# Optimization experiments

Measured on AMD Instinct MI355X. Metric: run time of the kernel, lower is better.

Reference implementation:

```python
import jax, jax.numpy as jnp
import numpy as np

TOP_K = 2
N_EXP = 64
EVAL_CAPACITY = 2.0


def setup_inputs() -> dict:
    key = jax.random.key(0)
    k1, k2 = jax.random.split(key)
    x = jax.random.normal(k1, (4, 4096, 2048), dtype=jnp.float32)
    w_g = jax.random.normal(k2, (N_EXP, 2048), dtype=jnp.float32) * 0.02  # Linear(n_embd, n_exp, bias=False)
    return {"x": x, "w_g": w_g}


def reference(x, w_g):
    B, T, C = x.shape
    num_tokens = B * T
    x_flat = x.reshape(num_tokens, C)
    # gating logits: [N, E]
    logits = jnp.einsum('nc,ec->ne', x_flat, w_g)
    # top-k selection
    top_k_logits, top_k_indices = jax.lax.top_k(logits, TOP_K)  # [N, k]
    router_probs = jax.nn.softmax(top_k_logits, axis=-1)        # [N, k]
    # static expert capacity (eval path)
    exp_capacity = max(int(TOP_K * EVAL_CAPACITY * num_tokens / N_EXP), 4)
    # one-hot expert mask [N, k, E]
    expert_mask = jax.nn.one_hot(top_k_indices, N_EXP, dtype=jnp.int32)
    # rank tokens within each expert via cumsum over (k-major, token) order
    reshaped = expert_mask.transpose(1, 0, 2).reshape(TOP_K * num_tokens, N_EXP)
    cumsum = jnp.cumsum(reshaped, axis=0)
    position = cumsum.reshape(TOP_K, num_tokens, N_EXP).transpose(1, 0, 2)  # [N, k, E]
    rank = (position - 1) * expert_mask
    capacity_mask = (rank < exp_capacity).astype(jnp.int32)
    final_mask = expert_mask * capacity_mask                     # [N, k, E]
    probs_mask = (final_mask.sum(axis=-1) > 0)                   # [N, k] bool
    router_probs_masked = router_probs * probs_mask.astype(router_probs.dtype)
    final_rank = rank.sum(axis=-1)                               # [N, k]
    return final_mask, router_probs_masked, top_k_indices, final_rank, exp_capacity
```

## Files before the change

### kernel.cpp

```cpp
#include <hip/hip_runtime.h>
#include <math.h>

#define C_DIM 2048
#define E_DIM 64
#define KC    128
#define BT    16
#define NW    4

typedef _Float16 h4    __attribute__((ext_vector_type(4)));
typedef _Float16 v8hf  __attribute__((ext_vector_type(8)));
typedef float    f32x4 __attribute__((ext_vector_type(4)));

#define SCALE      64.0f
#define INV_SCALE2 (1.0f/4096.0f)

__launch_bounds__(256)
__global__ void k_wsplit(const float* __restrict__ w, _Float16* __restrict__ wfrag)
{
    int t  = blockIdx.x * 256 + threadIdx.x;
    int l  = t & 63;
    int ni = (t >> 6) & 3;
    int q  = t >> 8;
    int e  = 16 * ni + (l & 15);
    int k0 = 32 * q + (l >> 4) * 8;
    const float* src = w + (size_t)e * C_DIM + k0;
    float4 a = *(const float4*)(src);
    float4 b = *(const float4*)(src + 4);
    float s[8] = {a.x, a.y, a.z, a.w, b.x, b.y, b.z, b.w};
    v8hf hv, lv;
#pragma unroll
    for (int j = 0; j < 8; ++j) {
        float sc = s[j] * SCALE;
        _Float16 h = (_Float16)sc;
        hv[j] = h;
        lv[j] = (_Float16)(sc - (float)h);
    }
    size_t fo = (size_t)(q * 4 + ni) * 2 * 512;
    *(v8hf*)(wfrag + fo + l * 8)       = hv;
    *(v8hf*)(wfrag + fo + 512 + l * 8) = lv;
}

__launch_bounds__(256, 4)
__global__ void k_logits_top2(const float* __restrict__ x, const _Float16* __restrict__ wfrag,
                              unsigned char* __restrict__ idx0, unsigned char* __restrict__ idx1,
                              float* __restrict__ dlt, unsigned short* __restrict__ gcounts,
                              int nblk)
{
    __shared__ alignas(16) char smem[2 * BT * KC * 2];

    const int tid  = threadIdx.x;
    const int lane = tid & 63;
    const int wk   = tid >> 6;
    const int ln15 = lane & 15;
    const int g    = lane >> 4;
    const int t0   = blockIdx.x * BT;

    f32x4 acc[4];
#pragma unroll
    for (int ni = 0; ni < 4; ++ni) acc[ni] = (f32x4)0.0f;

    float4 xr[2];

#define LOADX(kb)                                                              \
    {                                                                          \
        _Pragma("unroll")                                                      \
        for (int r = 0; r < 2; ++r) {                                          \
            int i = tid + 256 * r;                                             \
            int row = i >> 5, c4 = i & 31;                                     \
            xr[r] = *(const float4*)(x + (size_t)(t0 + row) * C_DIM + (kb) + c4 * 4); \
        }                                                                      \
    }

#define STOREX()                                                               \
    {                                                                          \
        _Pragma("unroll")                                                      \
        for (int r = 0; r < 2; ++r) {                                          \
            int i = tid + 256 * r;                                             \
            int row = i >> 5, c4 = i & 31;                                     \
            float4 v = xr[r];                                                  \
            float s0 = v.x * SCALE, s1 = v.y * SCALE, s2 = v.z * SCALE, s3 = v.w * SCALE; \
            _Float16 h0 = (_Float16)s0, h1 = (_Float16)s1, h2 = (_Float16)s2, h3 = (_Float16)s3; \
            h4 hv = {h0, h1, h2, h3};                                          \
            h4 lv = {(_Float16)(s0 - (float)h0), (_Float16)(s1 - (float)h1),   \
                     (_Float16)(s2 - (float)h2), (_Float16)(s3 - (float)h3)};  \
            int boff = row * 256 + ((c4 * 8) ^ ((row & 7) << 4));              \
            *(h4*)(smem + boff) = hv;                                          \
            *(h4*)(smem + 4096 + boff) = lv;                                   \
        }                                                                      \
    }

    LOADX(0);
    STOREX();
    __syncthreads();

    const int aoff = ln15 * 256 + (((wk << 6) + (g << 4)) ^ ((ln15 & 7) << 4));

    for (int c = 0; c < 16; ++c) {
        if (c < 15) LOADX((c + 1) * KC);

        const char* wp = (const char*)wfrag + ((size_t)(4 * c + wk) << 13) + (lane << 4);
        v8hf bh[4], bl[4];
#pragma unroll
        for (int ni = 0; ni < 4; ++ni) {
            bh[ni] = *(const v8hf*)(wp + (size_t)(2 * ni) * 1024);
            bl[ni] = *(const v8hf*)(wp + (size_t)(2 * ni) * 1024 + 1024);
        }
        v8hf ah = *(const v8hf*)(smem + aoff);
        v8hf al = *(const v8hf*)(smem + 4096 + aoff);

#pragma unroll
        for (int ni = 0; ni < 4; ++ni) {
            acc[ni] = __builtin_amdgcn_mfma_f32_16x16x32_f16(ah, bh[ni], acc[ni], 0, 0, 0);
            acc[ni] = __builtin_amdgcn_mfma_f32_16x16x32_f16(ah, bl[ni], acc[ni], 0, 0, 0);
            acc[ni] = __builtin_amdgcn_mfma_f32_16x16x32_f16(al, bh[ni], acc[ni], 0, 0, 0);
        }

        __syncthreads();
        if (c < 15) STOREX();
        __syncthreads();
    }

    float* lgs = (float*)smem;
    int*   cnt = (int*)(smem + 4096);
    if (tid < 128) cnt[tid] = 0;
#pragma unroll
    for (int w = 0; w < NW; ++w) {
        if (wk == w) {
#pragma unroll
            for (int ni = 0; ni < 4; ++ni)
#pragma unroll
                for (int gg = 0; gg < 4; ++gg) {
                    int row = (g << 2) + gg;
                    int e   = 16 * ni + ln15;
                    float vv = acc[ni][gg] * INV_SCALE2;
                    if (w == 0) lgs[row * 64 + e]  = vv;
                    else        lgs[row * 64 + e] += vv;
                }
        }
        __syncthreads();
    }

#pragma unroll
    for (int t = 0; t < 4; ++t) {
        int rowl = (wk << 2) + t;
        float v = lgs[rowl * 64 + lane];
        float vv = v; int ix = lane;
#pragma unroll
        for (int off = 32; off > 0; off >>= 1) {
            float ov = __shfl_down(vv, off, 64);
            int   oi = __shfl_down(ix, off, 64);
            if (ov > vv || (ov == vv && oi < ix)) { vv = ov; ix = oi; }
        }
        int   i1 = __shfl(ix, 0, 64);
        float v1 = __shfl(vv, 0, 64);

        vv = (lane == i1) ? -3.0e38f : v; ix = lane;
#pragma unroll
        for (int off = 32; off > 0; off >>= 1) {
            float ov = __shfl_down(vv, off, 64);
            int   oi = __shfl_down(ix, off, 64);
            if (ov > vv || (ov == vv && oi < ix)) { vv = ov; ix = oi; }
        }
        int   i2 = __shfl(ix, 0, 64);
        float v2 = __shfl(vv, 0, 64);

        if (lane == 0) {
            int n = t0 + rowl;
            idx0[n] = (unsigned char)i1;
            idx1[n] = (unsigned char)i2;
            dlt[n]  = v2 - v1;
            atomicAdd(&cnt[i1], 1);
            atomicAdd(&cnt[64 + i2], 1);
        }
    }

    __syncthreads();
    if (tid < 128) {
        int e = tid & 63, k = tid >> 6;
        gcounts[(size_t)e * (2 * nblk) + k * nblk + blockIdx.x] = (unsigned short)cnt[tid];
    }
}

__launch_bounds__(64)
__global__ void k_scan2(unsigned short* __restrict__ g, int S)
{
    const int e = blockIdx.x, lane = threadIdx.x;
    unsigned short* row = g + (size_t)e * S;
    int vals[32];
    const int R = S >> 6;
#pragma unroll
    for (int r = 0; r < 32; ++r) if (r < R) vals[r] = row[(r << 6) + lane];
    int running = 0;
#pragma unroll
    for (int r = 0; r < 32; ++r) {
        if (r >= R) break;
        int v = vals[r], s = v;
#pragma unroll
        for (int off = 1; off < 64; off <<= 1) {
            int t = __shfl_up(s, off, 64);
            if (lane >= off) s += t;
        }
        row[(r << 6) + lane] = (unsigned short)(s - v + running);
        running += __shfl(s, 63, 64);
    }
}

__launch_bounds__(128)
__global__ void k_rank_out(const unsigned char* __restrict__ idx0, const unsigned char* __restrict__ idx1,
                           const unsigned short* __restrict__ gpre, const float* __restrict__ dlt,
                           float* __restrict__ out, int N, int cap, int nblk)
{
    const int b = blockIdx.x, tid = threadIdx.x;
    const int lane = tid & 63, kk = tid >> 6;
    const int t0 = b * BT;
    __shared__ int sm_ix[2][BT], sm_rk[2][BT];

    int v = -1, base = 0;
    if (lane < BT) {
        v = (kk ? idx1 : idx0)[t0 + lane];
        base = gpre[(size_t)v * (2 * nblk) + kk * nblk + b];
    }
    const unsigned long long ltm = (1ull << lane) - 1ull;
    int pre = 0;
    for (int e = 0; e < 64; ++e) {
        unsigned long long bb = __ballot(v == e);
        if (v == e) pre = __popcll(bb & ltm);
    }
    if (lane < BT) { sm_ix[kk][lane] = v; sm_rk[kk][lane] = base + pre; }
    __syncthreads();

#pragma unroll
    for (int rep = 0; rep < 4; ++rep) {
        int f   = tid + 128 * rep;
        int n2  = f >> 5;
        int rem = (f & 31) * 4;
        int kq  = rem >> 6;
        int e0  = rem & 63;
        int ix  = sm_ix[kq][n2];
        int rr  = sm_rk[kq][n2];
        float val = (rr < cap) ? 1.0f : 0.0f;
        float4 o = make_float4(0.f, 0.f, 0.f, 0.f);
        int d = ix - e0;
        if (d >= 0 && d < 4) ((float*)&o)[d] = val;
        *(float4*)(out + (size_t)(t0 + n2) * 128 + rem) = o;
    }

    size_t B = (size_t)2 * N * E_DIM;
    if (tid < 2 * BT) {
        int n2 = tid >> 1, kq = tid & 1;
        int n  = t0 + n2;
        int gi = 2 * n + kq;
        int ix = sm_ix[kq][n2];
        int rr = sm_rk[kq][n2];
        float d  = dlt[n];
        float e1 = expf(d);
        float inv = 1.0f / (1.0f + e1);
        float p  = kq ? (e1 * inv) : inv;
        bool keep = rr < cap;
        out[B + gi]         = keep ? p : 0.0f;
        out[B + 2 * N + gi] = (float)ix;
        out[B + 4 * N + gi] = (float)rr;
    }
    if (b == 0 && tid == 0) out[B + 6 * N] = (float)cap;
}

extern "C" void kernel_launch(void* const* d_in, const int* in_sizes, int n_in,
                              void* d_out, int out_size, void* d_ws, size_t ws_size,
                              hipStream_t stream)
{
    const float* x  = (const float*)d_in[0];
    const float* wg = (const float*)d_in[1];
    const int N = in_sizes[0] / C_DIM;
    const int nblk = N / BT;

    char* ws = (char*)d_ws;
    unsigned char*  idx0    = (unsigned char*)ws;
    unsigned char*  idx1    = idx0 + N;
    float*          dlt     = (float*)(idx1 + N);
    unsigned short* gcounts = (unsigned short*)(dlt + N);
    _Float16*       wfrag   = (_Float16*)(gcounts + (size_t)64 * 2 * nblk);

    float* out = (float*)d_out;

    int cap = (int)((long long)2 * 2 * N / E_DIM);
    if (cap < 4) cap = 4;

    k_wsplit<<<64, 256, 0, stream>>>(wg, wfrag);
    k_logits_top2<<<nblk, 256, 0, stream>>>(x, wfrag, idx0, idx1, dlt, gcounts, nblk);
    k_scan2<<<E_DIM, 64, 0, stream>>>(gcounts, 2 * nblk);
    k_rank_out<<<nblk, 128, 0, stream>>>(idx0, idx1, gcounts, dlt, out, N, cap, nblk);
}
```

Baseline: 251.3 us.

## Double tokens per block, double-buffer LDS and prefetch weight fragments

Raises the token tile per block from 16 to 32, so each wave runs two M-subtiles that share the same weight fragments, halving weight reloads per token. The LDS staging buffer is now double-buffered, which removes one barrier per K-chunk, and the next chunk's weight fragments are prefetched into registers while the current chunk computes. The downstream scan and output kernels are resized to the new block count. The costs are higher register and LDS use, with the occupancy hint dropped from launch bounds, and half as many blocks in the grid.

```diff
diff --git a/kernel.cpp b/kernel.cpp
--- a/kernel.cpp
+++ b/kernel.cpp
@@ -4,7 +4,7 @@
 #define C_DIM 2048
 #define E_DIM 64
 #define KC    128
-#define BT    16
+#define BT    32
 #define NW    4
 
 typedef _Float16 h4    __attribute__((ext_vector_type(4)));
@@ -35,18 +35,18 @@
         hv[j] = h;
         lv[j] = (_Float16)(sc - (float)h);
     }
-    size_t fo = (size_t)(q * 4 + ni) * 2 * 512;
+    size_t fo = (size_t)(q * 4 + ni) * 1024;
     *(v8hf*)(wfrag + fo + l * 8)       = hv;
     *(v8hf*)(wfrag + fo + 512 + l * 8) = lv;
 }
 
-__launch_bounds__(256, 4)
+__launch_bounds__(256)
 __global__ void k_logits_top2(const float* __restrict__ x, const _Float16* __restrict__ wfrag,
                               unsigned char* __restrict__ idx0, unsigned char* __restrict__ idx1,
                               float* __restrict__ dlt, unsigned short* __restrict__ gcounts,
                               int nblk)
 {
-    __shared__ alignas(16) char smem[2 * BT * KC * 2];
+    __shared__ alignas(16) char smem[2 * 16384];
 
     const int tid  = threadIdx.x;
     const int lane = tid & 63;
@@ -55,94 +55,112 @@
     const int g    = lane >> 4;
     const int t0   = blockIdx.x * BT;
 
-    f32x4 acc[4];
-#pragma unroll
-    for (int ni = 0; ni < 4; ++ni) acc[ni] = (f32x4)0.0f;
-
-    float4 xr[2];
-
-#define LOADX(kb)                                                              \
-    {                                                                          \
-        _Pragma("unroll")                                                      \
-        for (int r = 0; r < 2; ++r) {                                          \
-            int i = tid + 256 * r;                                             \
-            int row = i >> 5, c4 = i & 31;                                     \
+    f32x4 acc[2][4];
+#pragma unroll
+    for (int mi = 0; mi < 2; ++mi)
+#pragma unroll
+        for (int ni = 0; ni < 4; ++ni) acc[mi][ni] = (f32x4)0.0f;
+
+    float4 xr[4];
+    v8hf bh[2][4], bl[2][4];
+
+#define LOADX(kb)                                                               \
+    {                                                                           \
+        _Pragma("unroll")                                                       \
+        for (int r = 0; r < 4; ++r) {                                           \
+            int i = tid + 256 * r;                                              \
+            int row = i >> 5, c4 = i & 31;                                      \
             xr[r] = *(const float4*)(x + (size_t)(t0 + row) * C_DIM + (kb) + c4 * 4); \
-        }                                                                      \
-    }
-
-#define STOREX()                                                               \
-    {                                                                          \
-        _Pragma("unroll")                                                      \
-        for (int r = 0; r < 2; ++r) {                                          \
-            int i = tid + 256 * r;                                             \
-            int row = i >> 5, c4 = i & 31;                                     \
-            float4 v = xr[r];                                                  \
+        }                                                                       \
+    }
+
+#define STOREX(bf)                                                              \
+    {                                                                           \
+        _Pragma("unroll")                                                       \
+        for (int r = 0; r < 4; ++r) {                                           \
+            int i = tid + 256 * r;                                              \
+            int row = i >> 5, c4 = i & 31;                                      \
+            float4 v = xr[r];                                                   \
             float s0 = v.x * SCALE, s1 = v.y * SCALE, s2 = v.z * SCALE, s3 = v.w * SCALE; \
             _Float16 h0 = (_Float16)s0, h1 = (_Float16)s1, h2 = (_Float16)s2, h3 = (_Float16)s3; \
-            h4 hv = {h0, h1, h2, h3};                                          \
-            h4 lv = {(_Float16)(s0 - (float)h0), (_Float16)(s1 - (float)h1),   \
-                     (_Float16)(s2 - (float)h2), (_Float16)(s3 - (float)h3)};  \
-            int boff = row * 256 + ((c4 * 8) ^ ((row & 7) << 4));              \
-            *(h4*)(smem + boff) = hv;                                          \
-            *(h4*)(smem + 4096 + boff) = lv;                                   \
-        }                                                                      \
+            h4 hv = {h0, h1, h2, h3};                                           \
+            h4 lv = {(_Float16)(s0 - (float)h0), (_Float16)(s1 - (float)h1),    \
+                     (_Float16)(s2 - (float)h2), (_Float16)(s3 - (float)h3)};   \
+            int boff = (bf) * 16384 + row * 256 + ((c4 * 8) ^ ((row & 7) << 4));\
+            *(h4*)(smem + boff)        = hv;                                    \
+            *(h4*)(smem + boff + 8192) = lv;                                    \
+        }                                                                       \
+    }
+
+#define LOADB(c, s)                                                             \
+    {                                                                           \
+        const char* wp = (const char*)wfrag + ((size_t)(4 * (c) + wk) << 13) + (lane << 4); \
+        _Pragma("unroll")                                                       \
+        for (int ni = 0; ni < 4; ++ni) {                                        \
+            bh[s][ni] = *(const v8hf*)(wp + ni * 2048);                         \
+            bl[s][ni] = *(const v8hf*)(wp + ni * 2048 + 1024);                  \
+        }                                                                       \
     }
 
     LOADX(0);
-    STOREX();
+    LOADB(0, 0);
+    STOREX(0);
     __syncthreads();
 
-    const int aoff = ln15 * 256 + (((wk << 6) + (g << 4)) ^ ((ln15 & 7) << 4));
-
+    const int sw   = (ln15 & 7) << 4;
+    const int koff = ((wk << 6) + (g << 4)) ^ sw;
+
+#pragma unroll
     for (int c = 0; c < 16; ++c) {
-        if (c < 15) LOADX((c + 1) * KC);
-
-        const char* wp = (const char*)wfrag + ((size_t)(4 * c + wk) << 13) + (lane << 4);
-        v8hf bh[4], bl[4];
-#pragma unroll
-        for (int ni = 0; ni < 4; ++ni) {
-            bh[ni] = *(const v8hf*)(wp + (size_t)(2 * ni) * 1024);
-            bl[ni] = *(const v8hf*)(wp + (size_t)(2 * ni) * 1024 + 1024);
-        }
-        v8hf ah = *(const v8hf*)(smem + aoff);
-        v8hf al = *(const v8hf*)(smem + 4096 + aoff);
-
-#pragma unroll
-        for (int ni = 0; ni < 4; ++ni) {
-            acc[ni] = __builtin_amdgcn_mfma_f32_16x16x32_f16(ah, bh[ni], acc[ni], 0, 0, 0);
-            acc[ni] = __builtin_amdgcn_mfma_f32_16x16x32_f16(ah, bl[ni], acc[ni], 0, 0, 0);
-            acc[ni] = __builtin_amdgcn_mfma_f32_16x16x32_f16(al, bh[ni], acc[ni], 0, 0, 0);
-        }
-
+        const int cur = c & 1, nxt = cur ^ 1;
+        if (c < 15) {
+            LOADX((c + 1) * KC);
+            LOADB(c + 1, nxt);
+        }
+        v8hf ah[2], al[2];
+#pragma unroll
+        for (int mi = 0; mi < 2; ++mi) {
+            int ro = cur * 16384 + (16 * mi + ln15) * 256 + koff;
+            ah[mi] = *(const v8hf*)(smem + ro);
+            al[mi] = *(const v8hf*)(smem + ro + 8192);
+        }
+#pragma unroll
+        for (int ni = 0; ni < 4; ++ni)
+#pragma unroll
+            for (int mi = 0; mi < 2; ++mi) {
+                acc[mi][ni] = __builtin_amdgcn_mfma_f32_16x16x32_f16(ah[mi], bh[cur][ni], acc[mi][ni], 0, 0, 0);
+                acc[mi][ni] = __builtin_amdgcn_mfma_f32_16x16x32_f16(ah[mi], bl[cur][ni], acc[mi][ni], 0, 0, 0);
+                acc[mi][ni] = __builtin_amdgcn_mfma_f32_16x16x32_f16(al[mi], bh[cur][ni], acc[mi][ni], 0, 0, 0);
+            }
+        if (c < 15) STOREX(nxt);
         __syncthreads();
-        if (c < 15) STOREX();
-        __syncthreads();
     }
 
     float* lgs = (float*)smem;
-    int*   cnt = (int*)(smem + 4096);
+    int*   cnt = (int*)(smem + 8192);
     if (tid < 128) cnt[tid] = 0;
 #pragma unroll
     for (int w = 0; w < NW; ++w) {
         if (wk == w) {
 #pragma unroll
-            for (int ni = 0; ni < 4; ++ni)
-#pragma unroll
-                for (int gg = 0; gg < 4; ++gg) {
-                    int row = (g << 2) + gg;
-                    int e   = 16 * ni + ln15;
-                    float vv = acc[ni][gg] * INV_SCALE2;
-                    if (w == 0) lgs[row * 64 + e]  = vv;
-                    else        lgs[row * 64 + e] += vv;
-                }
+            for (int mi = 0; mi < 2; ++mi)
+#pragma unroll
+                for (int ni = 0; ni < 4; ++ni)
+#pragma unroll
+                    for (int gg = 0; gg < 4; ++gg) {
+                        int row = 16 * mi + (g << 2) + gg;
+                        int e   = 16 * ni + ln15;
+                        float vv = acc[mi][ni][gg] * INV_SCALE2;
+                        if (w == 0) lgs[row * 64 + e]  = vv;
+                        else        lgs[row * 64 + e] += vv;
+                    }
         }
         __syncthreads();
     }
 
 #pragma unroll
-    for (int t = 0; t < 4; ++t) {
-        int rowl = (wk << 2) + t;
+    for (int t = 0; t < 8; ++t) {
+        int rowl = (wk << 3) + t;
         float v = lgs[rowl * 64 + lane];
         float vv = v; int ix = lane;
 #pragma unroll
@@ -186,13 +204,13 @@
 {
     const int e = blockIdx.x, lane = threadIdx.x;
     unsigned short* row = g + (size_t)e * S;
-    int vals[32];
+    int vals[16];
     const int R = S >> 6;
 #pragma unroll
-    for (int r = 0; r < 32; ++r) if (r < R) vals[r] = row[(r << 6) + lane];
+    for (int r = 0; r < 16; ++r) if (r < R) vals[r] = row[(r << 6) + lane];
     int running = 0;
 #pragma unroll
-    for (int r = 0; r < 32; ++r) {
+    for (int r = 0; r < 16; ++r) {
         if (r >= R) break;
         int v = vals[r], s = v;
 #pragma unroll
@@ -230,7 +248,7 @@
     __syncthreads();
 
 #pragma unroll
-    for (int rep = 0; rep < 4; ++rep) {
+    for (int rep = 0; rep < 8; ++rep) {
         int f   = tid + 128 * rep;
         int n2  = f >> 5;
         int rem = (f & 31) * 4;
```

Result: faster. 240.8 us (-4.2%).
